# Optimization experiments

Hardware: AMD Instinct MI355X
Metric: run time of the kernel (lower is better)

## Reference

```python
import jax, jax.numpy as jnp
import numpy as np

IN_F, OUT_F, TASK_D, RANK, HID = 1024, 1024, 256, 8, 64
ALPHA = 8.0
SCALING = ALPHA / RANK  # 1.0


def setup_inputs() -> dict:
    key = jax.random.key(0)
    ks = jax.random.split(key, 12)
    s = 0.02
    return {
        "x": jax.random.normal(ks[0], (4, 2048, IN_F), dtype=jnp.float32),
        "base_out": jax.random.normal(ks[1], (4, 2048, OUT_F), dtype=jnp.float32),
        "task_emb": jax.random.normal(ks[2], (4, TASK_D), dtype=jnp.float32),
        # gen_a MLP: Linear(task_dim->hid) + GELU + Linear(hid->out*r)
        "Wa1": jax.random.normal(ks[3], (HID, TASK_D), dtype=jnp.float32) * s,
        "ba1": jnp.zeros((HID,), dtype=jnp.float32),
        "Wa2": jax.random.normal(ks[4], (OUT_F * RANK, HID), dtype=jnp.float32) * s,
        "ba2": jnp.zeros((OUT_F * RANK,), dtype=jnp.float32),
        # gen_b MLP: Linear(task_dim->hid) + GELU + Linear(hid->r*in)
        "Wb1": jax.random.normal(ks[5], (HID, TASK_D), dtype=jnp.float32) * s,
        "bb1": jnp.zeros((HID,), dtype=jnp.float32),
        "Wb2": jax.random.normal(ks[6], (RANK * IN_F, HID), dtype=jnp.float32) * s,
        "bb2": jnp.zeros((RANK * IN_F,), dtype=jnp.float32),
    }


def reference(x, base_out, task_emb, Wa1, ba1, Wa2, ba2, Wb1, bb1, Wb2, bb2):
    lead = x.shape[:-1]
    x2d = x.reshape(-1, IN_F)                      # (b_eff, in)
    b_eff = x2d.shape[0]
    # broadcast task_emb to b_eff rows (repeat + trim, as in torch)
    B = task_emb.shape[0]
    reps = (b_eff + B - 1) // B
    task_eff = jnp.tile(task_emb, (reps, 1))[:b_eff]  # (b_eff, task_dim)

    gelu = lambda t: jax.nn.gelu(t, approximate=False)
    h_a = gelu(task_eff @ Wa1.T + ba1)
    vec_a = h_a @ Wa2.T + ba2                      # (b_eff, out*r)
    h_b = gelu(task_eff @ Wb1.T + bb1)
    vec_b = h_b @ Wb2.T + bb2                      # (b_eff, r*in)

    a = vec_a.reshape(b_eff, OUT_F, RANK)
    b = vec_b.reshape(b_eff, RANK, IN_F)

    # dropout p=0 (eval): x passes through
    tmp = jnp.einsum('bi,bri->br', x2d, b)         # (b_eff, r)
    y_delta = jnp.einsum('br,bor->bo', tmp, a)     # (b_eff, out)
    y = base_out.reshape(-1, OUT_F) + SCALING * y_delta
    return y.reshape(*lead, OUT_F)
```

## Files before the change

kernel.cpp:

```cpp
#include <hip/hip_runtime.h>
#include <math.h>

#define IN_F   1024
#define OUT_F  1024
#define TASK_D 256
#define RANK   8
#define HID    64

typedef float vfloat4 __attribute__((ext_vector_type(4)));

__device__ __forceinline__ float gelu_exact(float v) {
    return 0.5f * v * (1.0f + erff(v * 0.70710678118654752f));
}

__global__ __launch_bounds__(256) void gen_kernel(
    const float* __restrict__ task_emb,
    const float* __restrict__ Wa1, const float* __restrict__ ba1,
    const float* __restrict__ Wa2, const float* __restrict__ ba2,
    const float* __restrict__ Wb1, const float* __restrict__ bb1,
    const float* __restrict__ Wb2, const float* __restrict__ bb2,
    float* __restrict__ vec_a_t, float* __restrict__ vec_b)
{
    const int gen = blockIdx.x >> 7;
    const int blk = blockIdx.x & 127;
    const float* __restrict__ W1 = gen ? Wb1 : Wa1;
    const float* __restrict__ b1 = gen ? bb1 : ba1;
    const float* __restrict__ W2 = gen ? Wb2 : Wa2;
    const float* __restrict__ b2 = gen ? bb2 : ba2;

    __shared__ float hs[4][HID];
    {
        const int j = threadIdx.x >> 2;
        const int t = threadIdx.x & 3;
        const float4* te = (const float4*)(task_emb + t * TASK_D);
        const float4* w  = (const float4*)(W1 + j * TASK_D);
        float acc = 0.f;
        #pragma unroll
        for (int d = 0; d < TASK_D / 4; ++d) {
            float4 a = te[d], b = w[d];
            acc += a.x * b.x + a.y * b.y + a.z * b.z + a.w * b.w;
        }
        hs[t][j] = gelu_exact(acc + b1[j]);
    }
    __syncthreads();

    const int lrow = threadIdx.x >> 2;
    const int q    = threadIdx.x & 3;
    const int o    = blk * 64 + lrow;

    const float4* w2 = (const float4*)(W2 + (size_t)o * HID + q * 16);
    float acc0 = 0.f, acc1 = 0.f, acc2 = 0.f, acc3 = 0.f;
    #pragma unroll
    for (int k = 0; k < 4; ++k) {
        float4 w = w2[k];
        const int kb = q * 16 + k * 4;
        acc0 += hs[0][kb] * w.x + hs[0][kb+1] * w.y + hs[0][kb+2] * w.z + hs[0][kb+3] * w.w;
        acc1 += hs[1][kb] * w.x + hs[1][kb+1] * w.y + hs[1][kb+2] * w.z + hs[1][kb+3] * w.w;
        acc2 += hs[2][kb] * w.x + hs[2][kb+1] * w.y + hs[2][kb+2] * w.z + hs[2][kb+3] * w.w;
        acc3 += hs[3][kb] * w.x + hs[3][kb+1] * w.y + hs[3][kb+2] * w.z + hs[3][kb+3] * w.w;
    }
    #pragma unroll
    for (int off = 1; off <= 2; off <<= 1) {
        acc0 += __shfl_xor(acc0, off, 64);
        acc1 += __shfl_xor(acc1, off, 64);
        acc2 += __shfl_xor(acc2, off, 64);
        acc3 += __shfl_xor(acc3, off, 64);
    }
    if (q == 0) {
        const float bb = b2[o];
        float v[4] = { acc0 + bb, acc1 + bb, acc2 + bb, acc3 + bb };
        if (gen == 0) {
            const int oo = o >> 3, r = o & 7;
            #pragma unroll
            for (int t = 0; t < 4; ++t)
                vec_a_t[t * (RANK * OUT_F) + r * OUT_F + oo] = v[t];
        } else {
            #pragma unroll
            for (int t = 0; t < 4; ++t)
                vec_b[t * (RANK * IN_F) + o] = v[t];
        }
    }
}

__global__ __launch_bounds__(256, 4) void apply_kernel(
    const float* __restrict__ x, const float* __restrict__ base_out,
    const float* __restrict__ vec_a_t, const float* __restrict__ vec_b,
    float* __restrict__ out)
{
    const int t    = blockIdx.x & 3;
    const int g    = blockIdx.x >> 2;
    const int wave = threadIdx.x >> 6;
    const int lane = threadIdx.x & 63;

    const int j    = g * 8 + wave * 2;
    const int row0 = t + 4 * j;
    const int row1 = row0 + 4;

    __shared__ float bs[RANK * IN_F];

    vfloat4 stage[8];
    {
        const vfloat4* src = (const vfloat4*)(vec_b + (size_t)t * (RANK * IN_F));
        #pragma unroll
        for (int i = 0; i < 8; ++i)
            stage[i] = src[threadIdx.x + 256 * i];
    }

    vfloat4 xv[2][4], bo[2][4];
    {
        const float* __restrict__ xr0 = x + (size_t)row0 * IN_F;
        const float* __restrict__ xr1 = x + (size_t)row1 * IN_F;
        const float* __restrict__ br0 = base_out + (size_t)row0 * OUT_F;
        const float* __restrict__ br1 = base_out + (size_t)row1 * OUT_F;
        #pragma unroll
        for (int c = 0; c < 4; ++c) {
            const int k = c * 256 + lane * 4;
            xv[0][c] = __builtin_nontemporal_load((const vfloat4*)(xr0 + k));
            xv[1][c] = __builtin_nontemporal_load((const vfloat4*)(xr1 + k));
            bo[0][c] = __builtin_nontemporal_load((const vfloat4*)(br0 + k));
            bo[1][c] = __builtin_nontemporal_load((const vfloat4*)(br1 + k));
        }
    }

    {
        vfloat4* dst = (vfloat4*)bs;
        #pragma unroll
        for (int i = 0; i < 8; ++i)
            dst[threadIdx.x + 256 * i] = stage[i];
    }
    __syncthreads();

    float acc[2][RANK];
    #pragma unroll
    for (int i = 0; i < 2; ++i)
        #pragma unroll
        for (int r = 0; r < RANK; ++r) acc[i][r] = 0.f;

    #pragma unroll
    for (int c = 0; c < 4; ++c) {
        const int k = c * 256 + lane * 4;
        #pragma unroll
        for (int r = 0; r < RANK; ++r) {
            const float4 bv = *(const float4*)(bs + r * IN_F + k);
            acc[0][r] += xv[0][c].x * bv.x + xv[0][c].y * bv.y
                       + xv[0][c].z * bv.z + xv[0][c].w * bv.w;
            acc[1][r] += xv[1][c].x * bv.x + xv[1][c].y * bv.y
                       + xv[1][c].z * bv.z + xv[1][c].w * bv.w;
        }
    }

    #pragma unroll
    for (int off = 32; off > 0; off >>= 1) {
        #pragma unroll
        for (int i = 0; i < 2; ++i)
            #pragma unroll
            for (int r = 0; r < RANK; ++r)
                acc[i][r] += __shfl_xor(acc[i][r], off, 64);
    }

    const float* __restrict__ at = vec_a_t + (size_t)t * (RANK * OUT_F);
    float* __restrict__ or0 = out + (size_t)row0 * OUT_F;
    float* __restrict__ or1 = out + (size_t)row1 * OUT_F;

    #pragma unroll
    for (int c = 0; c < 4; ++c) {
        const int o = c * 256 + lane * 4;
        float4 af[RANK];
        #pragma unroll
        for (int r = 0; r < RANK; ++r)
            af[r] = *(const float4*)(at + r * OUT_F + o);

        vfloat4 rv0 = bo[0][c];
        vfloat4 rv1 = bo[1][c];
        #pragma unroll
        for (int r = 0; r < RANK; ++r) {
            rv0.x += acc[0][r] * af[r].x;  rv0.y += acc[0][r] * af[r].y;
            rv0.z += acc[0][r] * af[r].z;  rv0.w += acc[0][r] * af[r].w;
            rv1.x += acc[1][r] * af[r].x;  rv1.y += acc[1][r] * af[r].y;
            rv1.z += acc[1][r] * af[r].z;  rv1.w += acc[1][r] * af[r].w;
        }
        __builtin_nontemporal_store(rv0, (vfloat4*)(or0 + o));
        __builtin_nontemporal_store(rv1, (vfloat4*)(or1 + o));
    }
}

extern "C" void kernel_launch(void* const* d_in, const int* in_sizes, int n_in,
                              void* d_out, int out_size, void* d_ws, size_t ws_size,
                              hipStream_t stream) {
    const float* x        = (const float*)d_in[0];
    const float* base_out = (const float*)d_in[1];
    const float* task_emb = (const float*)d_in[2];
    const float* Wa1      = (const float*)d_in[3];
    const float* ba1      = (const float*)d_in[4];
    const float* Wa2      = (const float*)d_in[5];
    const float* ba2      = (const float*)d_in[6];
    const float* Wb1      = (const float*)d_in[7];
    const float* bb1      = (const float*)d_in[8];
    const float* Wb2      = (const float*)d_in[9];
    const float* bb2      = (const float*)d_in[10];
    float* out = (float*)d_out;

    float* vec_a_t = (float*)d_ws;
    float* vec_b   = vec_a_t + 4 * RANK * OUT_F;

    const int b_eff = in_sizes[0] / IN_F;

    gen_kernel<<<256, 256, 0, stream>>>(task_emb, Wa1, ba1, Wa2, ba2,
                                        Wb1, bb1, Wb2, bb2, vec_a_t, vec_b);
    apply_kernel<<<b_eff / 8, 256, 0, stream>>>(x, base_out, vec_a_t, vec_b, out);
}
```

Measured before the change: 147.2 us.

## Process four rows per wave in apply kernel to amortize LDS staging

Each wave now handles four rows instead of two, halving the grid so the 32KB vec_b copy staged into shared memory serves twice as many rows. The base_out load moves after the reduction, and nontemporal loads and stores become plain accesses. Launch bounds drop to 2 blocks per CU to make room for the extra registers. The cost is fewer blocks in flight, less latency hiding, and base_out loads no longer overlapped with the x loads.

```diff
diff --git a/kernel.cpp b/kernel.cpp
--- a/kernel.cpp
+++ b/kernel.cpp
@@ -82,7 +82,7 @@
     }
 }
 
-__global__ __launch_bounds__(256, 4) void apply_kernel(
+__global__ __launch_bounds__(256, 2) void apply_kernel(
     const float* __restrict__ x, const float* __restrict__ base_out,
     const float* __restrict__ vec_a_t, const float* __restrict__ vec_b,
     float* __restrict__ out)
@@ -92,9 +92,7 @@
     const int wave = threadIdx.x >> 6;
     const int lane = threadIdx.x & 63;
 
-    const int j    = g * 8 + wave * 2;
-    const int row0 = t + 4 * j;
-    const int row1 = row0 + 4;
+    const int jb   = g * 16 + wave * 4;
 
     __shared__ float bs[RANK * IN_F];
 
@@ -106,20 +104,13 @@
             stage[i] = src[threadIdx.x + 256 * i];
     }
 
-    vfloat4 xv[2][4], bo[2][4];
-    {
-        const float* __restrict__ xr0 = x + (size_t)row0 * IN_F;
-        const float* __restrict__ xr1 = x + (size_t)row1 * IN_F;
-        const float* __restrict__ br0 = base_out + (size_t)row0 * OUT_F;
-        const float* __restrict__ br1 = base_out + (size_t)row1 * OUT_F;
-        #pragma unroll
-        for (int c = 0; c < 4; ++c) {
-            const int k = c * 256 + lane * 4;
-            xv[0][c] = __builtin_nontemporal_load((const vfloat4*)(xr0 + k));
-            xv[1][c] = __builtin_nontemporal_load((const vfloat4*)(xr1 + k));
-            bo[0][c] = __builtin_nontemporal_load((const vfloat4*)(br0 + k));
-            bo[1][c] = __builtin_nontemporal_load((const vfloat4*)(br1 + k));
-        }
+    float4 xv[4][4];
+    #pragma unroll
+    for (int i = 0; i < 4; ++i) {
+        const float* __restrict__ xr = x + (size_t)(t + 4 * (jb + i)) * IN_F;
+        #pragma unroll
+        for (int c = 0; c < 4; ++c)
+            xv[i][c] = *(const float4*)(xr + c * 256 + lane * 4);
     }
 
     {
@@ -130,9 +121,9 @@
     }
     __syncthreads();
 
-    float acc[2][RANK];
-    #pragma unroll
-    for (int i = 0; i < 2; ++i)
+    float acc[4][RANK];
+    #pragma unroll
+    for (int i = 0; i < 4; ++i)
         #pragma unroll
         for (int r = 0; r < RANK; ++r) acc[i][r] = 0.f;
 
@@ -142,25 +133,33 @@
         #pragma unroll
         for (int r = 0; r < RANK; ++r) {
             const float4 bv = *(const float4*)(bs + r * IN_F + k);
-            acc[0][r] += xv[0][c].x * bv.x + xv[0][c].y * bv.y
-                       + xv[0][c].z * bv.z + xv[0][c].w * bv.w;
-            acc[1][r] += xv[1][c].x * bv.x + xv[1][c].y * bv.y
-                       + xv[1][c].z * bv.z + xv[1][c].w * bv.w;
+            #pragma unroll
+            for (int i = 0; i < 4; ++i) {
+                acc[i][r] += xv[i][c].x * bv.x + xv[i][c].y * bv.y
+                           + xv[i][c].z * bv.z + xv[i][c].w * bv.w;
+            }
         }
     }
 
     #pragma unroll
     for (int off = 32; off > 0; off >>= 1) {
         #pragma unroll
-        for (int i = 0; i < 2; ++i)
+        for (int i = 0; i < 4; ++i)
             #pragma unroll
             for (int r = 0; r < RANK; ++r)
                 acc[i][r] += __shfl_xor(acc[i][r], off, 64);
     }
 
     const float* __restrict__ at = vec_a_t + (size_t)t * (RANK * OUT_F);
-    float* __restrict__ or0 = out + (size_t)row0 * OUT_F;
-    float* __restrict__ or1 = out + (size_t)row1 * OUT_F;
+
+    float4 bo[4][4];
+    #pragma unroll
+    for (int i = 0; i < 4; ++i) {
+        const float* __restrict__ br = base_out + (size_t)(t + 4 * (jb + i)) * OUT_F;
+        #pragma unroll
+        for (int c = 0; c < 4; ++c)
+            bo[i][c] = *(const float4*)(br + c * 256 + lane * 4);
+    }
 
     #pragma unroll
     for (int c = 0; c < 4; ++c) {
@@ -170,17 +169,18 @@
         for (int r = 0; r < RANK; ++r)
             af[r] = *(const float4*)(at + r * OUT_F + o);
 
-        vfloat4 rv0 = bo[0][c];
-        vfloat4 rv1 = bo[1][c];
-        #pragma unroll
-        for (int r = 0; r < RANK; ++r) {
-            rv0.x += acc[0][r] * af[r].x;  rv0.y += acc[0][r] * af[r].y;
-            rv0.z += acc[0][r] * af[r].z;  rv0.w += acc[0][r] * af[r].w;
-            rv1.x += acc[1][r] * af[r].x;  rv1.y += acc[1][r] * af[r].y;
-            rv1.z += acc[1][r] * af[r].z;  rv1.w += acc[1][r] * af[r].w;
-        }
-        __builtin_nontemporal_store(rv0, (vfloat4*)(or0 + o));
-        __builtin_nontemporal_store(rv1, (vfloat4*)(or1 + o));
+        #pragma unroll
+        for (int i = 0; i < 4; ++i) {
+            float4 rv = bo[i][c];
+            #pragma unroll
+            for (int r = 0; r < RANK; ++r) {
+                rv.x += acc[i][r] * af[r].x;
+                rv.y += acc[i][r] * af[r].y;
+                rv.z += acc[i][r] * af[r].z;
+                rv.w += acc[i][r] * af[r].w;
+            }
+            *(float4*)(out + (size_t)(t + 4 * (jb + i)) * OUT_F + o) = rv;
+        }
     }
 }
 
@@ -207,5 +207,5 @@
 
     gen_kernel<<<256, 256, 0, stream>>>(task_emb, Wa1, ba1, Wa2, ba2,
                                         Wb1, bb1, Wb2, bb2, vec_a_t, vec_b);
-    apply_kernel<<<b_eff / 8, 256, 0, stream>>>(x, base_out, vec_a_t, vec_b, out);
-}
+    apply_kernel<<<b_eff / 16, 256, 0, stream>>>(x, base_out, vec_a_t, vec_b, out);
+}
```

After: 146.6 us. Within noise of the previous version (-0.4%).
